# Optimization experiments

Hardware: AMD Instinct MI355X
Metric: run time of the kernel (lower is better)

## Reference

```python
import jax, jax.numpy as jnp
import numpy as np
import math

B, T, C, H = 4, 2048, 768, 12
HS = C // H  # 64


def setup_inputs() -> dict:
    key = jax.random.key(0)
    ks = jax.random.split(key, 6)
    s = 1.0 / math.sqrt(C)
    return {
        "x": jax.random.normal(ks[0], (B, T, C), dtype=jnp.float32),
        "memory": jax.random.normal(ks[1], (B, T, C), dtype=jnp.float32),
        "Wq": jax.random.normal(ks[2], (C, C), dtype=jnp.float32) * s,
        "bq": jnp.zeros((C,), dtype=jnp.float32),
        "Wkv": jax.random.normal(ks[3], (C, 2 * C), dtype=jnp.float32) * s,
        "bkv": jnp.zeros((2 * C,), dtype=jnp.float32),
        "Wproj": jax.random.normal(ks[4], (C, C), dtype=jnp.float32) * s,
        "bproj": jnp.zeros((C,), dtype=jnp.float32),
    }


def reference(x, memory, Wq, bq, Wkv, bkv, Wproj, bproj):
    # q projection of decoder stream x, kv projection of encoder memory
    q = x @ Wq + bq                      # [B,T,C]
    kv = memory @ Wkv + bkv              # [B,T,2C]
    k, v = jnp.split(kv, 2, axis=2)      # [B,T,C] each

    def heads(t):
        return t.reshape(B, T, H, HS).transpose(0, 2, 1, 3)  # [B,H,T,hs]

    q, k, v = heads(q), heads(k), heads(v)
    scale = 1.0 / math.sqrt(HS)
    att = jnp.einsum("bhqd,bhkd->bhqk", q, k) * scale        # [B,H,T,T]
    att = jax.nn.softmax(att, axis=-1)
    y = jnp.einsum("bhqk,bhkd->bhqd", att, v)                # [B,H,T,hs]
    y = y.transpose(0, 2, 1, 3).reshape(B, T, C)
    return y @ Wproj + bproj
```

## Files before the change

### kernel.cpp

```cpp
#include <hip/hip_runtime.h>
#include <hip/hip_bf16.h>


#define B_  4
#define T_  2048
#define C_  768
#define H_  12
#define HS_ 64

typedef __attribute__((ext_vector_type(8))) short short8;
typedef __attribute__((ext_vector_type(4))) float f32x4;

__device__ __forceinline__ short f2bf(float f) {
    __hip_bfloat16 h = __float2bfloat16(f);
    return *reinterpret_cast<short*>(&h);
}

__device__ __forceinline__ unsigned cvtpk(float lo, float hi) {
    unsigned r;
    asm("v_cvt_pk_bf16_f32 %0, %1, %2" : "=v"(r) : "v"(lo), "v"(hi));
    return r;
}

__device__ __forceinline__ void gload_lds16(const void* g, void* l) {
    __builtin_amdgcn_global_load_lds((const __attribute__((address_space(1))) void*)g,
                                     (__attribute__((address_space(3))) void*)l,
                                     16, 0, 0);
}


__global__ void prepass(const float* __restrict__ x, short* __restrict__ xb,
                        const float* __restrict__ mem, short* __restrict__ memb,
                        const float* __restrict__ Wq,  short* __restrict__ WqT,
                        const float* __restrict__ Wkv, short* __restrict__ WkvT,
                        const float* __restrict__ Wp,  short* __restrict__ WpT,
                        float qscale) {
    const int n4 = 8192 * 768 / 4;
    const int cvtblocks = (2 * n4) / 256;
    int bid = blockIdx.x;
    if (bid < cvtblocks) {
        int i = bid * 256 + threadIdx.x;
        const float* in; short* out;
        if (i < n4) { in = x; out = xb; }
        else        { in = mem; out = memb; i -= n4; }
        float4 v = reinterpret_cast<const float4*>(in)[i];
        short4 o;
        o.x = f2bf(v.x); o.y = f2bf(v.y); o.z = f2bf(v.z); o.w = f2bf(v.w);
        reinterpret_cast<short4*>(out)[i] = o;
        return;
    }
    __shared__ float tile[32][33];
    bid -= cvtblocks;
    const float* in; short* out; int N; float sc = 1.0f;
    if (bid < 576)       { in = Wq;  out = WqT;  N = 768;  sc = qscale; }
    else if (bid < 1728) { in = Wkv; out = WkvT; N = 1536; bid -= 576; }
    else                 { in = Wp;  out = WpT;  N = 768;  bid -= 1728; }
    const int tiles_n = N >> 5;
    const int k0 = (bid / tiles_n) * 32;
    const int n0 = (bid % tiles_n) * 32;
    const int r = threadIdx.x >> 5;
    const int c = threadIdx.x & 31;
    #pragma unroll
    for (int i = 0; i < 4; ++i)
        tile[r + 8 * i][c] = in[(size_t)(k0 + r + 8 * i) * N + n0 + c];
    __syncthreads();
    #pragma unroll
    for (int i = 0; i < 4; ++i)
        out[(size_t)(n0 + r + 8 * i) * 768 + k0 + c] = f2bf(tile[c][r + 8 * i] * sc);
}


template<int OUT_F32, int WRITE_KV>
__device__ __forceinline__ void gemm_body(const short* __restrict__ A, const short* __restrict__ BT,
                                          const float* __restrict__ bias, void* __restrict__ out,
                                          short* __restrict__ kt, short* __restrict__ vt,
                                          int m0, int n0, int K, int ldo, float bscale,
                                          short (*As)[64], short (*Bs)[64]) {
    const int t  = threadIdx.x;
    const int wid = t >> 6;
    const int wm = wid >> 1, wn = wid & 1;
    const int lane = t & 63;
    const int lr = lane & 15;
    const int lk = (lane >> 4) * 8;

    f32x4 acc[4][4] = {};

    const int srow = wid * 32 + (lane >> 3);
    const int scol = (lane & 7) * 8;

    for (int k0 = 0; k0 < K; k0 += 64) {
        __syncthreads();
        #pragma unroll
        for (int i = 0; i < 4; ++i)
            gload_lds16(&A[(size_t)(m0 + srow + i * 8) * K + k0 + scol],
                        &As[wid * 32 + i * 8][0]);
        #pragma unroll
        for (int i = 0; i < 4; ++i)
            gload_lds16(&BT[(size_t)(n0 + srow + i * 8) * K + k0 + scol],
                        &Bs[wid * 32 + i * 8][0]);
        __syncthreads();

        #pragma unroll
        for (int ks = 0; ks < 2; ++ks) {
            const int kk = ks * 32 + lk;
            short8 a[4], b[4];
            #pragma unroll
            for (int m = 0; m < 4; ++m)
                a[m] = *reinterpret_cast<const short8*>(&As[wm*64 + m*16 + lr][kk]);
            #pragma unroll
            for (int n = 0; n < 4; ++n)
                b[n] = *reinterpret_cast<const short8*>(&Bs[wn*64 + n*16 + lr][kk]);
            #pragma unroll
            for (int m = 0; m < 4; ++m)
                #pragma unroll
                for (int n = 0; n < 4; ++n)
                    acc[m][n] = __builtin_amdgcn_mfma_f32_16x16x32_bf16(a[m], b[n], acc[m][n], 0, 0, 0);
        }
    }

    const int rb = m0 + wm * 64;
    const int cb = n0 + wn * 64;
    const int rj = (lane >> 4) * 4;
    #pragma unroll
    for (int n = 0; n < 4; ++n) {
        const int col = cb + n * 16 + lr;
        const float bv = bias[col] * bscale;
        #pragma unroll
        for (int m = 0; m < 4; ++m) {
            #pragma unroll
            for (int j = 0; j < 4; ++j) {
                const int row = rb + m * 16 + rj + j;
                const float v = acc[m][n][j] + bv;
                if (WRITE_KV) {
                    const int bb = row >> 11, tt = row & 2047;
                    if (col < 768) {
                        const int hh = col >> 6, dd = col & 63;
                        const int s = ((((dd >> 3) ^ (tt & 7)) << 3) | (dd & 7));
                        kt[(((size_t)bb * H_ + hh) * T_ + tt) * 64 + s] = f2bf(v);
                    } else {
                        const int vd = col - 768;
                        const int hh = vd >> 6, dd = vd & 63;
                        const int kv = tt & 63;
                        const int slot = 32 * (kv >> 5) + 8 * ((kv >> 2) & 3)
                                       + 4 * ((kv >> 4) & 1) + (kv & 3);
                        const int slot2 = (((slot >> 3) ^ (dd & 7)) << 3) | (slot & 7);
                        vt[(((size_t)bb * H_ + hh) * HS_ + dd) * T_ + (tt & ~63) + slot2] = f2bf(v);
                    }
                } else if (OUT_F32) {
                    reinterpret_cast<float*>(out)[(size_t)row * ldo + col] = v;
                } else {
                    reinterpret_cast<short*>(out)[(size_t)row * ldo + col] = f2bf(v);
                }
            }
        }
    }
}

__global__ void gemm_qkv(const short* __restrict__ xb,  const short* __restrict__ memb,
                         const short* __restrict__ WqT, const short* __restrict__ WkvT,
                         const float* __restrict__ bq,  const float* __restrict__ bkv,
                         short* __restrict__ qb, short* __restrict__ kt,
                         short* __restrict__ vt, float qscale) {
    __shared__ short As[128][64];
    __shared__ short Bs[128][64];
    const int lin = blockIdx.y * 18 + blockIdx.x;
    const int swz = (lin % 8) * 144 + lin / 8;
    const int bx = swz % 18;
    const int m0 = (swz / 18) * 128;
    if (bx < 6) {
        gemm_body<0,0>(xb, WqT, bq, qb, nullptr, nullptr, m0, bx * 128, 768, 768, qscale, As, Bs);
    } else {
        gemm_body<0,1>(memb, WkvT, bkv, nullptr, kt, vt, m0, (bx - 6) * 128, 768, 1536, 1.0f, As, Bs);
    }
}

__global__ void gemm_out(const short* __restrict__ yb, const short* __restrict__ WpT,
                         const float* __restrict__ bproj, float* __restrict__ out) {
    __shared__ short As[128][64];
    __shared__ short Bs[128][64];
    const int lin = blockIdx.y * 6 + blockIdx.x;
    const int swz = (lin % 8) * 48 + lin / 8;
    gemm_body<1,0>(yb, WpT, bproj, out, nullptr, nullptr, (swz / 6) * 128, (swz % 6) * 128,
                   768, 768, 1.0f, As, Bs);
}


__global__ void __launch_bounds__(256)
attn_fwd20(const short* __restrict__ qb, const short* __restrict__ ktb,
           const short* __restrict__ vtb, short* __restrict__ yb) {
    __shared__ short Ks[2][64][72];
    __shared__ short Vt[2][64][72];

    const int id = blockIdx.x;
    const int pair = id % 48;
    const int b = pair / H_, h = pair % H_;
    const int q0 = (id / 48) * 128;
    const int t = threadIdx.x;
    const int w = t >> 6;
    const int lane = t & 63;
    const int lr = lane & 15;
    const int g = lane >> 4;

    const int str = t >> 2;
    const int stc = (t & 3) * 16;
    const int x8  = str & 7;
    const int wc0 = (((stc >> 3) ^ x8) << 3);
    const int wc1 = ((((stc >> 3) + 1) ^ x8) << 3);

    const short* Kb = ktb + (size_t)(b * H_ + h) * T_ * 64;
    const short* Vb = vtb + (size_t)(b * H_ + h) * HS_ * T_;

    short8 aq[2][2];
    #pragma unroll
    for (int m = 0; m < 2; ++m)
        #pragma unroll
        for (int ks = 0; ks < 2; ++ks)
            aq[m][ks] = *reinterpret_cast<const short8*>(
                &qb[(size_t)(b * T_ + q0 + w * 32 + m * 16 + lr) * C_ + h * HS_ + ks * 32 + g * 8]);

    short8 ones8;
    #pragma unroll
    for (int i = 0; i < 8; ++i) ones8[i] = (short)0x3F80;
    const f32x4 z4 = {0.f, 0.f, 0.f, 0.f};

    f32x4 acc[2][4] = {};
    f32x4 accl[2] = {};

    uint4 kr0, kr1, vr0, vr1;
    {
        const short* gk = &Kb[(size_t)str * 64 + stc];
        const short* gv = &Vb[(size_t)str * T_ + stc];
        kr0 = *reinterpret_cast<const uint4*>(gk);
        kr1 = *reinterpret_cast<const uint4*>(gk + 8);
        vr0 = *reinterpret_cast<const uint4*>(gv);
        vr1 = *reinterpret_cast<const uint4*>(gv + 8);
    }

    int c = 0;
    for (int kv0 = 0; kv0 < T_; kv0 += 64) {
        *reinterpret_cast<uint4*>(&Ks[c][str][wc0]) = kr0;
        *reinterpret_cast<uint4*>(&Ks[c][str][wc1]) = kr1;
        *reinterpret_cast<uint4*>(&Vt[c][str][wc0]) = vr0;
        *reinterpret_cast<uint4*>(&Vt[c][str][wc1]) = vr1;

        if (kv0 + 64 < T_) {
            const short* gk = &Kb[(size_t)(kv0 + 64 + str) * 64 + stc];
            const short* gv = &Vb[(size_t)str * T_ + kv0 + 64 + stc];
            kr0 = *reinterpret_cast<const uint4*>(gk);
            kr1 = *reinterpret_cast<const uint4*>(gk + 8);
            vr0 = *reinterpret_cast<const uint4*>(gv);
            vr1 = *reinterpret_cast<const uint4*>(gv + 8);
        }

        __syncthreads();

        f32x4 s[2][4];
        #pragma unroll
        for (int n = 0; n < 4; ++n) {
            short8 bk = *reinterpret_cast<const short8*>(&Ks[c][n * 16 + lr][g * 8]);
            #pragma unroll
            for (int m = 0; m < 2; ++m)
                s[m][n] = __builtin_amdgcn_mfma_f32_16x16x32_bf16(bk, aq[m][0], z4, 0, 0, 0);
        }
        #pragma unroll
        for (int n = 0; n < 4; ++n) {
            short8 bk = *reinterpret_cast<const short8*>(&Ks[c][n * 16 + lr][32 + g * 8]);
            #pragma unroll
            for (int m = 0; m < 2; ++m)
                s[m][n] = __builtin_amdgcn_mfma_f32_16x16x32_bf16(bk, aq[m][1], s[m][n], 0, 0, 0);
        }

        short8 pa[2][2];
        #pragma unroll
        for (int m = 0; m < 2; ++m) {
            #pragma unroll
            for (int n = 0; n < 4; ++n) {
                #pragma unroll
                for (int j = 0; j < 4; ++j)
                    s[m][n][j] = exp2f(s[m][n][j]);
            }
            #pragma unroll
            for (int ks = 0; ks < 2; ++ks) {
                uint4 u;
                u.x = cvtpk(s[m][2*ks][0],   s[m][2*ks][1]);
                u.y = cvtpk(s[m][2*ks][2],   s[m][2*ks][3]);
                u.z = cvtpk(s[m][2*ks+1][0], s[m][2*ks+1][1]);
                u.w = cvtpk(s[m][2*ks+1][2], s[m][2*ks+1][3]);
                pa[m][ks] = __builtin_bit_cast(short8, u);
            }
        }

        #pragma unroll
        for (int ks = 0; ks < 2; ++ks) {
            #pragma unroll
            for (int m = 0; m < 2; ++m)
                accl[m] = __builtin_amdgcn_mfma_f32_16x16x32_bf16(pa[m][ks], ones8, accl[m], 0, 0, 0);
            #pragma unroll
            for (int n = 0; n < 4; ++n) {
                short8 bv = *reinterpret_cast<const short8*>(&Vt[c][n * 16 + lr][ks * 32 + g * 8]);
                #pragma unroll
                for (int m = 0; m < 2; ++m)
                    acc[m][n] = __builtin_amdgcn_mfma_f32_16x16x32_bf16(pa[m][ks], bv, acc[m][n], 0, 0, 0);
            }
        }

        c ^= 1;
    }

    #pragma unroll
    for (int m = 0; m < 2; ++m) {
        #pragma unroll
        for (int j = 0; j < 4; ++j) {
            const float inv = 1.f / accl[m][j];
            const size_t row = (size_t)(b * T_ + q0 + w * 32 + m * 16 + g * 4 + j);
            #pragma unroll
            for (int n = 0; n < 4; ++n)
                yb[row * C_ + h * HS_ + n * 16 + lr] = f2bf(acc[m][n][j] * inv);
        }
    }
}


extern "C" void kernel_launch(void* const* d_in, const int* in_sizes, int n_in,
                              void* d_out, int out_size, void* d_ws, size_t ws_size,
                              hipStream_t stream) {
    const float* x      = (const float*)d_in[0];
    const float* memory = (const float*)d_in[1];
    const float* Wq     = (const float*)d_in[2];
    const float* bq     = (const float*)d_in[3];
    const float* Wkv    = (const float*)d_in[4];
    const float* bkv    = (const float*)d_in[5];
    const float* Wproj  = (const float*)d_in[6];
    const float* bproj  = (const float*)d_in[7];

    char* ws = (char*)d_ws;
    size_t off = 0;
    auto alloc = [&](size_t bytes) { char* p = ws + off; off += (bytes + 255) & ~(size_t)255; return p; };
    short* xb   = (short*)alloc((size_t)8192 * 768 * 2);
    short* memb = (short*)alloc((size_t)8192 * 768 * 2);
    short* qb   = (short*)alloc((size_t)8192 * 768 * 2);
    short* ktb  = (short*)alloc((size_t)B_ * H_ * T_ * 64 * 2);
    short* vtb  = (short*)alloc((size_t)B_ * H_ * HS_ * T_ * 2);
    short* WqT  = (short*)alloc((size_t)768 * 768 * 2);
    short* WkvT = (short*)alloc((size_t)1536 * 768 * 2);
    short* WpT  = (short*)alloc((size_t)768 * 768 * 2);

    const float qscale = 1.4426950408889634f / 8.0f;

    prepass<<<12288 + 2304, 256, 0, stream>>>(x, xb, memory, memb,
                                              Wq, WqT, Wkv, WkvT, Wproj, WpT, qscale);
    gemm_qkv<<<dim3(18, 64), 256, 0, stream>>>(xb, memb, WqT, WkvT, bq, bkv, qb, ktb, vtb, qscale);
    attn_fwd20<<<dim3(16 * 48), 256, 0, stream>>>(qb, ktb, vtb, xb );
    gemm_out<<<dim3(6, 64), 256, 0, stream>>>(xb, WpT, bproj, (float*)d_out);
}
```

Baseline: 167.0 us.

## Use two waves per attention block with 64 query rows per wave

The attention kernel now launches 128 threads (two waves) per block instead of four, and each wave handles 64 query rows instead of 32. The block still covers 128 queries, so each K/V tile in shared memory feeds twice as many MFMAs per wave, and each LDS B-fragment read is reused across four M tiles instead of two. Staging is redistributed so each thread loads four 16-byte chunks of K and of V. The cost is much higher register pressure (acc doubles to 16 f32x4 plus 16 score tiles), which may reduce occupancy or cause spills.

```diff
diff --git a/kernel.cpp b/kernel.cpp
--- a/kernel.cpp
+++ b/kernel.cpp
@@ -185,8 +185,8 @@
 }
 
 
-__global__ void __launch_bounds__(256)
-attn_fwd20(const short* __restrict__ qb, const short* __restrict__ ktb,
+__global__ void __launch_bounds__(128)
+attn_fwd21(const short* __restrict__ qb, const short* __restrict__ ktb,
            const short* __restrict__ vtb, short* __restrict__ yb) {
     __shared__ short Ks[2][64][72];
     __shared__ short Vt[2][64][72];
@@ -201,78 +201,79 @@
     const int lr = lane & 15;
     const int g = lane >> 4;
 
-    const int str = t >> 2;
-    const int stc = (t & 3) * 16;
+    const int str = t >> 1;
+    const int stc = (t & 1) * 32;
     const int x8  = str & 7;
-    const int wc0 = (((stc >> 3) ^ x8) << 3);
-    const int wc1 = ((((stc >> 3) + 1) ^ x8) << 3);
+    int wc[4];
+    #pragma unroll
+    for (int i = 0; i < 4; ++i)
+        wc[i] = ((((stc >> 3) + i) ^ x8) << 3);
 
     const short* Kb = ktb + (size_t)(b * H_ + h) * T_ * 64;
     const short* Vb = vtb + (size_t)(b * H_ + h) * HS_ * T_;
 
-    short8 aq[2][2];
-    #pragma unroll
-    for (int m = 0; m < 2; ++m)
+    short8 aq[4][2];
+    #pragma unroll
+    for (int m = 0; m < 4; ++m)
         #pragma unroll
         for (int ks = 0; ks < 2; ++ks)
             aq[m][ks] = *reinterpret_cast<const short8*>(
-                &qb[(size_t)(b * T_ + q0 + w * 32 + m * 16 + lr) * C_ + h * HS_ + ks * 32 + g * 8]);
+                &qb[(size_t)(b * T_ + q0 + w * 64 + m * 16 + lr) * C_ + h * HS_ + ks * 32 + g * 8]);
 
     short8 ones8;
     #pragma unroll
     for (int i = 0; i < 8; ++i) ones8[i] = (short)0x3F80;
     const f32x4 z4 = {0.f, 0.f, 0.f, 0.f};
 
-    f32x4 acc[2][4] = {};
-    f32x4 accl[2] = {};
-
-    uint4 kr0, kr1, vr0, vr1;
-    {
-        const short* gk = &Kb[(size_t)str * 64 + stc];
-        const short* gv = &Vb[(size_t)str * T_ + stc];
-        kr0 = *reinterpret_cast<const uint4*>(gk);
-        kr1 = *reinterpret_cast<const uint4*>(gk + 8);
-        vr0 = *reinterpret_cast<const uint4*>(gv);
-        vr1 = *reinterpret_cast<const uint4*>(gv + 8);
+    f32x4 acc[4][4] = {};
+    f32x4 accl[4] = {};
+
+    uint4 kr[4], vr[4];
+    #pragma unroll
+    for (int i = 0; i < 4; ++i) {
+        kr[i] = *reinterpret_cast<const uint4*>(&Kb[(size_t)str * 64 + stc + 8 * i]);
+        vr[i] = *reinterpret_cast<const uint4*>(&Vb[(size_t)str * T_ + stc + 8 * i]);
     }
 
     int c = 0;
     for (int kv0 = 0; kv0 < T_; kv0 += 64) {
-        *reinterpret_cast<uint4*>(&Ks[c][str][wc0]) = kr0;
-        *reinterpret_cast<uint4*>(&Ks[c][str][wc1]) = kr1;
-        *reinterpret_cast<uint4*>(&Vt[c][str][wc0]) = vr0;
-        *reinterpret_cast<uint4*>(&Vt[c][str][wc1]) = vr1;
+        #pragma unroll
+        for (int i = 0; i < 4; ++i) {
+            *reinterpret_cast<uint4*>(&Ks[c][str][wc[i]]) = kr[i];
+            *reinterpret_cast<uint4*>(&Vt[c][str][wc[i]]) = vr[i];
+        }
 
         if (kv0 + 64 < T_) {
-            const short* gk = &Kb[(size_t)(kv0 + 64 + str) * 64 + stc];
-            const short* gv = &Vb[(size_t)str * T_ + kv0 + 64 + stc];
-            kr0 = *reinterpret_cast<const uint4*>(gk);
-            kr1 = *reinterpret_cast<const uint4*>(gk + 8);
-            vr0 = *reinterpret_cast<const uint4*>(gv);
-            vr1 = *reinterpret_cast<const uint4*>(gv + 8);
+            #pragma unroll
+            for (int i = 0; i < 4; ++i) {
+                kr[i] = *reinterpret_cast<const uint4*>(
+                    &Kb[(size_t)(kv0 + 64 + str) * 64 + stc + 8 * i]);
+                vr[i] = *reinterpret_cast<const uint4*>(
+                    &Vb[(size_t)str * T_ + kv0 + 64 + stc + 8 * i]);
+            }
         }
 
         __syncthreads();
 
-        f32x4 s[2][4];
+        f32x4 s[4][4];
         #pragma unroll
         for (int n = 0; n < 4; ++n) {
             short8 bk = *reinterpret_cast<const short8*>(&Ks[c][n * 16 + lr][g * 8]);
             #pragma unroll
-            for (int m = 0; m < 2; ++m)
+            for (int m = 0; m < 4; ++m)
                 s[m][n] = __builtin_amdgcn_mfma_f32_16x16x32_bf16(bk, aq[m][0], z4, 0, 0, 0);
         }
         #pragma unroll
         for (int n = 0; n < 4; ++n) {
             short8 bk = *reinterpret_cast<const short8*>(&Ks[c][n * 16 + lr][32 + g * 8]);
             #pragma unroll
-            for (int m = 0; m < 2; ++m)
+            for (int m = 0; m < 4; ++m)
                 s[m][n] = __builtin_amdgcn_mfma_f32_16x16x32_bf16(bk, aq[m][1], s[m][n], 0, 0, 0);
         }
 
-        short8 pa[2][2];
-        #pragma unroll
-        for (int m = 0; m < 2; ++m) {
+        short8 pa[4][2];
+        #pragma unroll
+        for (int m = 0; m < 4; ++m) {
             #pragma unroll
             for (int n = 0; n < 4; ++n) {
                 #pragma unroll
@@ -293,13 +294,13 @@
         #pragma unroll
         for (int ks = 0; ks < 2; ++ks) {
             #pragma unroll
-            for (int m = 0; m < 2; ++m)
+            for (int m = 0; m < 4; ++m)
                 accl[m] = __builtin_amdgcn_mfma_f32_16x16x32_bf16(pa[m][ks], ones8, accl[m], 0, 0, 0);
             #pragma unroll
             for (int n = 0; n < 4; ++n) {
                 short8 bv = *reinterpret_cast<const short8*>(&Vt[c][n * 16 + lr][ks * 32 + g * 8]);
                 #pragma unroll
-                for (int m = 0; m < 2; ++m)
+                for (int m = 0; m < 4; ++m)
                     acc[m][n] = __builtin_amdgcn_mfma_f32_16x16x32_bf16(pa[m][ks], bv, acc[m][n], 0, 0, 0);
             }
         }
@@ -308,11 +309,11 @@
     }
 
     #pragma unroll
-    for (int m = 0; m < 2; ++m) {
+    for (int m = 0; m < 4; ++m) {
         #pragma unroll
         for (int j = 0; j < 4; ++j) {
             const float inv = 1.f / accl[m][j];
-            const size_t row = (size_t)(b * T_ + q0 + w * 32 + m * 16 + g * 4 + j);
+            const size_t row = (size_t)(b * T_ + q0 + w * 64 + m * 16 + g * 4 + j);
             #pragma unroll
             for (int n = 0; n < 4; ++n)
                 yb[row * C_ + h * HS_ + n * 16 + lr] = f2bf(acc[m][n][j] * inv);
@@ -350,6 +351,6 @@
     prepass<<<12288 + 2304, 256, 0, stream>>>(x, xb, memory, memb,
                                               Wq, WqT, Wkv, WkvT, Wproj, WpT, qscale);
     gemm_qkv<<<dim3(18, 64), 256, 0, stream>>>(xb, memb, WqT, WkvT, bq, bkv, qb, ktb, vtb, qscale);
-    attn_fwd20<<<dim3(16 * 48), 256, 0, stream>>>(qb, ktb, vtb, xb );
+    attn_fwd21<<<dim3(16 * 48), 128, 0, stream>>>(qb, ktb, vtb, xb );
     gemm_out<<<dim3(6, 64), 256, 0, stream>>>(xb, WpT, bproj, (float*)d_out);
 }
```

New measurement: 225.9 us. 35.3% more time.
